# Kernel optimization log

Measured on AMD Instinct MI355X. Metric: run time of the kernel, lower is better.

Reference implementation:

```python
import jax, jax.numpy as jnp
import numpy as np

N_TOKEN = 100000
D = 1024  # d_embed == d_model == d_proj
CUTOFFS = [0, 20000, 60000, 100000]  # cutoff_ends
N_SEQ = 2048


def setup_inputs() -> dict:
    key = jax.random.key(0)
    ks = jax.random.split(key, 20)
    w = lambda k, s: jax.random.normal(k, s, dtype=jnp.float32) * 0.02
    return {
        "x": jax.random.randint(ks[0], (N_SEQ,), 0, N_TOKEN),
        "labels": jax.random.randint(ks[1], (N_SEQ,), 0, N_TOKEN),
        # adaptive embedding tables (d_emb_i = 1024 / 4**i) and projections [d_proj, d_emb_i]
        "emb_w0": w(ks[2], (20000, 1024)),
        "emb_w1": w(ks[3], (40000, 256)),
        "emb_w2": w(ks[4], (40000, 64)),
        "emb_proj0": w(ks[5], (1024, 1024)),
        "emb_proj1": w(ks[6], (1024, 256)),
        "emb_proj2": w(ks[7], (1024, 64)),
        # adaptive softmax output layers + projections
        "out_w0": w(ks[8], (20000, 1024)),
        "out_b0": jnp.zeros((20000,), jnp.float32),
        "out_w1": w(ks[9], (40000, 256)),
        "out_b1": jnp.zeros((40000,), jnp.float32),
        "out_w2": w(ks[10], (40000, 64)),
        "out_b2": jnp.zeros((40000,), jnp.float32),
        "out_proj0": w(ks[11], (1024, 1024)),
        "out_proj1": w(ks[12], (1024, 256)),
        "out_proj2": w(ks[13], (1024, 64)),
        # cluster head tokens (one per tail cluster)
        "cluster_w": w(ks[14], (2, 1024)),
        "cluster_b": jnp.zeros((2,), jnp.float32),
    }


def _forward(x, labels,
             emb_w0, emb_w1, emb_w2, emb_proj0, emb_proj1, emb_proj2,
             out_w0, out_b0, out_w1, out_b1, out_w2, out_b2,
             out_proj0, out_proj1, out_proj2, cluster_w, cluster_b):
    scale = jnp.asarray(D ** 0.5, jnp.float32)
    # AdaptiveEmbedding (div_val>1): per-cluster embed -> project to d_proj, scatter by range.
    # Equivalent vectorized form: build the full projected table once, then gather.
    table = jnp.concatenate([
        emb_w0 @ emb_proj0.T,   # [20000, D]
        emb_w1 @ emb_proj1.T,   # [40000, D]
        emb_w2 @ emb_proj2.T,   # [40000, D]
    ], axis=0)                   # [N_TOKEN, D]
    hidden = table[x] * scale    # [N, D]

    n = hidden.shape[0]
    rows = jnp.arange(n)

    # Head: cluster-0 vocab + one logit per tail cluster.
    head_w = jnp.concatenate([out_w0, cluster_w], axis=0)   # [20002, D]
    head_b = jnp.concatenate([out_b0, cluster_b], axis=0)   # [20002]
    head_logit = (hidden @ out_proj0) @ head_w.T + head_b   # [N, 20002]
    head_lp = jax.nn.log_softmax(head_logit, axis=-1)
    head_size = head_lp.shape[1]

    # Cluster 0: direct lookup in the head.
    lp0 = head_lp[rows, jnp.clip(labels, 0, CUTOFFS[1] - 1)]

    # Tail clusters: dense per-cluster log-softmax, gathered at shifted target,
    # plus the head cluster-token logprob (original TXL uses column -i).
    def tail(w, b, proj, i):
        l, r = CUTOFFS[i], CUTOFFS[i + 1]
        tail_lp = jax.nn.log_softmax((hidden @ proj) @ w.T + b, axis=-1)  # [N, r-l]
        t = jnp.clip(labels - l, 0, r - l - 1)
        return head_lp[:, head_size - i] + tail_lp[rows, t]

    lp1 = tail(out_w1, out_b1, out_proj1, 1)
    lp2 = tail(out_w2, out_b2, out_proj2, 2)

    logprob = jnp.where(labels < CUTOFFS[1], lp0,
               jnp.where(labels < CUTOFFS[2], lp1, lp2))
    return -logprob  # nll, [N]


def reference(x, labels,
              emb_w0, emb_w1, emb_w2, emb_proj0, emb_proj1, emb_proj2,
              out_w0, out_b0, out_w1, out_b1, out_w2, out_b2,
              out_proj0, out_proj1, out_proj2, cluster_w, cluster_b):
    return _forward(x, labels,
                    emb_w0, emb_w1, emb_w2, emb_proj0, emb_proj1, emb_proj2,
                    out_w0, out_b0, out_w1, out_b1, out_w2, out_b2,
                    out_proj0, out_proj1, out_proj2, cluster_w, cluster_b)
```

## Files before the change

kernel.cpp:

```cpp
#include <hip/hip_runtime.h>

typedef _Float16 f16x8 __attribute__((ext_vector_type(8)));
typedef _Float16 f16x4 __attribute__((ext_vector_type(4)));
typedef float f32x4 __attribute__((ext_vector_type(4)));
typedef int i32x4 __attribute__((ext_vector_type(4)));
typedef int i32x8 __attribute__((ext_vector_type(8)));
typedef unsigned char u8;

#define DEVI __device__ __forceinline__

constexpr int NROWS = 2048;
constexpr int HEADV = 20002;
constexpr int HEADP = 20480;
constexpr int NCBH  = 160;
constexpr int PSTH  = 160;
constexpr int VT    = 40000;
constexpr int VTP   = 40320;
constexpr int NCBT  = 315;
constexpr int PSTT  = 320;

DEVI void glds16(const void* g, void* l) {
  __builtin_amdgcn_global_load_lds((const __attribute__((address_space(1))) unsigned int*)g,
                                   (__attribute__((address_space(3))) unsigned int*)l,
                                   16, 0, 0);
}

#define SIG(r) (((r) >> 1) & 7)
DEVI int swzb(int b, int r) {
  return (b & ~127) | ((((b >> 4) & 7) ^ SIG(r)) << 4) | (b & 15);
}

DEVI unsigned int to_e4m3(float f) {
  unsigned u = __float_as_uint(f);
  unsigned s = (u >> 24) & 0x80u;
  float a = fabsf(f);
  if (!(a < 448.f)) return s | 0x7E;
  if (a < 0.00097656f) return s;
  int exp = (int)((u >> 23) & 0xFF) - 127;
  int qexp = exp < -6 ? -6 : exp;
  int n = __float2int_rn(a * exp2f((float)(3 - qexp)));
  if (n >= 16) { qexp++; n = 8; }
  return s | (unsigned)(n < 8 ? n : (((qexp + 7) << 3) | (n - 8)));
}

DEVI float fr8(unsigned b) {
  unsigned e = (b >> 3) & 15u, m = b & 7u;
  float v;
  if (e) v = __uint_as_float(((e + 120u) << 23) | (m << 20));
  else   v = (float)m * 0.001953125f;
  return (b & 0x80u) ? -v : v;
}

__global__ void prep_par(const int* __restrict__ x, const int* __restrict__ labels,
                         int* cl, int* headcol, int* tailpos, int* pos1, int* pos2,
                         int* L1, int* L2, int* T0, int* T1, int* T2, int* counts)
{
  int n = blockIdx.x * 256 + threadIdx.x;
  int l = labels[n];
  int c = l < 20000 ? 0 : (l < 60000 ? 1 : 2);
  cl[n] = c;
  headcol[n] = c == 0 ? l : (c == 1 ? 20001 : 20000);
  tailpos[n] = c == 1 ? l - 20000 : (c == 2 ? l - 60000 : 0);
  if (c == 1) { int s = atomicAdd(&counts[0], 1); pos1[n] = s; L1[s] = n; }
  else if (c == 2) { int s = atomicAdd(&counts[1], 1); pos2[n] = s; L2[s] = n; }
  int t = x[n];
  int tc = t < 20000 ? 0 : (t < 60000 ? 1 : 2);
  int s = atomicAdd(&counts[2 + tc], 1);
  (tc == 0 ? T0 : tc == 1 ? T1 : T2)[s] = n;
}

constexpr int PB_A = HEADP * 1024 / 8 / 256;
constexpr int PB_B = PB_A + VTP * 256 / 8 / 256;
constexpr int PB_C = PB_B + VTP * 128 / 8 / 256;
constexpr int PB_D = PB_C + 1024;
constexpr int PB_E = PB_D + 256;
constexpr int PB_F = PB_E + 64;
constexpr int PB_G = PB_F + 1024;
constexpr int PB_H = PB_G + 256;
constexpr int PB_I = PB_H + 128;

DEVI void cvt_f16(const float* src, _Float16* dst, int vb, int tid) {
  int g = vb * 256 + tid;
  float4 v = *(const float4*)(src + (size_t)g * 4);
  f16x4 o = {(_Float16)v.x, (_Float16)v.y, (_Float16)v.z, (_Float16)v.w};
  *(f16x4*)(dst + (size_t)g * 4) = o;
}

DEVI void tr32(const float* in, _Float16* out, int C, int bx, int by, int tid) {
  __shared__ float tile[32][33];
  int c0 = bx * 32, r0 = by * 32;
  int tx = tid & 31, ty = tid >> 5;
  for (int i = 0; i < 4; i++) {
    int c = c0 + tx; int r = r0 + ty + i * 8;
    tile[ty + i * 8][tx] = (c < C) ? in[(size_t)r * C + c] : 0.f;
  }
  __syncthreads();
  for (int i = 0; i < 4; i++)
    out[(size_t)(c0 + ty + i * 8) * 1024 + r0 + tx] = (_Float16)tile[tx][ty + i * 8];
}

DEVI unsigned long pack8(const float* v) {
  unsigned long p = 0;
  #pragma unroll
  for (int j = 0; j < 8; j++) p |= (unsigned long)to_e4m3(v[j] * 64.f) << (8 * j);
  return p;
}

__global__ void fused_pack(const float* __restrict__ out_w0, const float* __restrict__ out_b0,
                           const float* __restrict__ cluster_w, const float* __restrict__ cluster_b,
                           const float* __restrict__ out_w1, const float* __restrict__ out_b1,
                           const float* __restrict__ out_w2, const float* __restrict__ out_b2,
                           const float* __restrict__ emb_proj0, const float* __restrict__ emb_proj1,
                           const float* __restrict__ emb_proj2,
                           const float* __restrict__ out_proj0, const float* __restrict__ out_proj1,
                           const float* __restrict__ out_proj2,
                           u8* headw, float* headb,
                           u8* w1q, float* b1p, u8* w2q, float* b2p,
                           _Float16* ep0f, _Float16* ep1f, _Float16* ep2f,
                           _Float16* op0T, _Float16* op1T, _Float16* op2T,
                           int* lists, int* counts)
{
  int bid = blockIdx.x, tid = threadIdx.x;
  int zi = bid * 256 + tid;
  if (zi < 5 * 2048) lists[zi] = 0;
  if (bid == 41 && tid < 8) counts[tid] = 0;
  if (bid < PB_A) {
    int g = bid * 256 + tid;
    int r = g >> 7, sl = g & 127;
    float v[8] = {};
    if (r < 20000) {
      *(float4*)v = *(const float4*)(out_w0 + (size_t)r * 1024 + sl * 8);
      *(float4*)(v + 4) = *(const float4*)(out_w0 + (size_t)r * 1024 + sl * 8 + 4);
    } else if (r < 20002) {
      *(float4*)v = *(const float4*)(cluster_w + (size_t)(r - 20000) * 1024 + sl * 8);
      *(float4*)(v + 4) = *(const float4*)(cluster_w + (size_t)(r - 20000) * 1024 + sl * 8 + 4);
    }
    *(unsigned long*)(headw + (size_t)r * 1024 + swzb(sl * 8, r)) = pack8(v);
    if (g < HEADP) headb[g] = g < 20000 ? out_b0[g] : (g < HEADV ? cluster_b[g - 20000] : -1e30f);
  } else if (bid < PB_B) {
    int g = (bid - PB_A) * 256 + tid;
    int r = g >> 5, sl = g & 31;
    float v[8] = {};
    if (r < VT) {
      *(float4*)v = *(const float4*)(out_w1 + (size_t)r * 256 + sl * 8);
      *(float4*)(v + 4) = *(const float4*)(out_w1 + (size_t)r * 256 + sl * 8 + 4);
    }
    *(unsigned long*)(w1q + (size_t)r * 256 + swzb(sl * 8, r)) = pack8(v);
    if (g < VTP) b1p[g] = g < VT ? out_b1[g] : -1e30f;
  } else if (bid < PB_C) {
    int g = (bid - PB_B) * 256 + tid;
    int r = g >> 4, sl = g & 15;
    float v[8] = {};
    if (r < VT && sl < 8) {
      *(float4*)v = *(const float4*)(out_w2 + (size_t)r * 64 + sl * 8);
      *(float4*)(v + 4) = *(const float4*)(out_w2 + (size_t)r * 64 + sl * 8 + 4);
    }
    *(unsigned long*)(w2q + (size_t)r * 128 + swzb(sl * 8, r)) = pack8(v);
    if (g < VTP) b2p[g] = g < VT ? out_b2[g] : -1e30f;
  } else if (bid < PB_D) { cvt_f16(emb_proj0, ep0f, bid - PB_C, tid); }
  else if (bid < PB_E) { cvt_f16(emb_proj1, ep1f, bid - PB_D, tid); }
  else if (bid < PB_F) { cvt_f16(emb_proj2, ep2f, bid - PB_E, tid); }
  else if (bid < PB_G) { int l = bid - PB_F; tr32(out_proj0, op0T, 1024, l & 31, l >> 5, tid); }
  else if (bid < PB_H) { int l = bid - PB_G; tr32(out_proj1, op1T, 256, l & 7, l >> 3, tid); }
  else                 { int l = bid - PB_H; tr32(out_proj2, op2T, 64, l & 3, l >> 2, tid); }
}

DEVI void gat(const float* emb, const int* x, const int* list, _Float16* dst,
              int tbase, int vmax, int log2E, int vb, int tid) {
  int g = vb * 256 + tid;
  int r = g >> (log2E - 2);
  int e4 = (g & ((1 << (log2E - 2)) - 1)) << 2;
  int n = list[r];
  int tl = x[n] - tbase;
  tl = tl < 0 ? 0 : (tl >= vmax ? vmax - 1 : tl);
  float4 v = *(const float4*)(emb + ((size_t)tl << log2E) + e4);
  f16x4 o = {(_Float16)(v.x * 32.f), (_Float16)(v.y * 32.f),
             (_Float16)(v.z * 32.f), (_Float16)(v.w * 32.f)};
  *(f16x4*)(dst + ((size_t)r << log2E) + e4) = o;
}

__global__ void fused_gather(const float* __restrict__ emb_w0, const float* __restrict__ emb_w1,
                             const float* __restrict__ emb_w2, const int* __restrict__ x,
                             const int* __restrict__ T0, const int* __restrict__ T1,
                             const int* __restrict__ T2,
                             _Float16* E0, _Float16* E1, _Float16* E2)
{
  int bid = blockIdx.x, tid = threadIdx.x;
  if (bid < 2048)      gat(emb_w0, x, T0, E0, 0, 20000, 10, bid, tid);
  else if (bid < 2560) gat(emb_w1, x, T1, E1, 20000, 40000, 8, bid - 2048, tid);
  else                 gat(emb_w2, x, T2, E2, 60000, 40000, 6, bid - 2560, tid);
}

struct Seg128 {
  const _Float16* A; int lda;
  const _Float16* Wm; int ldw;
  _Float16* C; int ldc; int Nvalid;
  u8* Cq; int ldq;
  const int* amap; const int* cmap; const int* cnt;
  int K; int nblk;
};

DEVI void gemm128_body(const Seg128& s, int rb, int cb) {
  int valid = s.cnt ? *s.cnt : NROWS;
  if (rb * 128 >= valid) return;
  __shared__ __attribute__((aligned(16))) _Float16 As[128 * 32];
  __shared__ __attribute__((aligned(16))) _Float16 Ws[128 * 32];
  int tid = threadIdx.x;
  int lane = tid & 63, wid = tid >> 6;
  int wr = wid >> 1, wc = wid & 1;
  int sr = wid * 32 + (lane >> 2);
  int arow0 = rb * 128 + sr, arow1 = arow0 + 16;
  if (s.amap) { arow0 = s.amap[arow0]; arow1 = s.amap[arow1]; }
  int ko = (lane & 3) * 8;
  const _Float16* ag0 = s.A + (size_t)arow0 * s.lda + ko;
  const _Float16* ag1 = s.A + (size_t)arow1 * s.lda + ko;
  const _Float16* wg0 = s.Wm + (size_t)(cb * 128 + sr) * s.ldw + ko;
  const _Float16* wg1 = wg0 + (size_t)16 * s.ldw;
  _Float16* as0 = As + (wid * 32) * 32;
  _Float16* as1 = as0 + 16 * 32;
  _Float16* ws0 = Ws + (wid * 32) * 32;
  _Float16* ws1 = ws0 + 16 * 32;
  f32x4 acc[4][4] = {};
  int lr = lane & 15, lk = (lane >> 4) * 8;
  const int nk = s.K >> 5;
  for (int kt = 0; kt < nk; ++kt) {
    int kofs = kt * 32;
    glds16(ag0 + kofs, as0);
    glds16(ag1 + kofs, as1);
    glds16(wg0 + kofs, ws0);
    glds16(wg1 + kofs, ws1);
    __syncthreads();
    f16x8 af[4], bf[4];
    #pragma unroll
    for (int mi = 0; mi < 4; mi++)
      af[mi] = *(const f16x8*)(As + (wr * 64 + mi * 16 + lr) * 32 + lk);
    #pragma unroll
    for (int ni = 0; ni < 4; ni++)
      bf[ni] = *(const f16x8*)(Ws + (wc * 64 + ni * 16 + lr) * 32 + lk);
    #pragma unroll
    for (int mi = 0; mi < 4; mi++)
      #pragma unroll
      for (int ni = 0; ni < 4; ni++)
        acc[mi][ni] = __builtin_amdgcn_mfma_f32_16x16x32_f16(af[mi], bf[ni], acc[mi][ni], 0, 0, 0);
    __syncthreads();
  }
  #pragma unroll
  for (int mi = 0; mi < 4; mi++) {
    #pragma unroll
    for (int j = 0; j < 4; j++) {
      int rl = wr * 64 + mi * 16 + (lane >> 4) * 4 + j;
      int rg = rb * 128 + rl;
      if (rg >= valid) continue;
      int orow = s.cmap ? s.cmap[rg] : rg;
      #pragma unroll
      for (int ni = 0; ni < 4; ni++) {
        int col = cb * 128 + wc * 64 + ni * 16 + (lane & 15);
        if (col < s.Nvalid) {
          float v = acc[mi][ni][j];
          s.C[(size_t)orow * s.ldc + col] = (_Float16)v;
          if (s.Cq) s.Cq[(size_t)orow * s.ldq + swzb(col, orow)] = (u8)to_e4m3(v * 8.f);
        }
      }
    }
  }
}

__global__ __launch_bounds__(256)
void gemm128_multi(Seg128 s0, Seg128 s1, Seg128 s2) {
  int b = blockIdx.x;
  if (b < s0.nblk)                    { gemm128_body(s0, b & 15, b >> 4); }
  else if (b < s0.nblk + s1.nblk)     { b -= s0.nblk; gemm128_body(s1, b & 15, b >> 4); }
  else                                { b -= s0.nblk + s1.nblk; gemm128_body(s2, b & 15, b >> 4); }
}

struct SegL {
  const u8* A; const u8* W; const float* bias; const int* cnt;
  float* pm; float* ps; int pstride; int K; int nrb; int nblk;
};

__global__ __launch_bounds__(256, 3)
void gemm_lse8_multi(SegL s0, SegL s1, SegL s2)
{
  __shared__ __attribute__((aligned(16))) u8 As[16384];
  __shared__ __attribute__((aligned(16))) u8 Ws[16384];

  int b = blockIdx.x;
  SegL s;
  if (b < s0.nblk) s = s0;
  else if (b < s0.nblk + s1.nblk) { s = s1; b -= s0.nblk; }
  else { s = s2; b -= s0.nblk + s1.nblk; }

  int q = s.nblk >> 3;
  int w = (b & 7) * q + (b >> 3);
  int rb = w % s.nrb, cb = w / s.nrb;
  int valid = s.cnt ? *s.cnt : NROWS;
  if (rb * 128 >= valid) return;

  const int K = s.K;
  int tid = threadIdx.x;
  int lane = tid & 63, wid = tid >> 6;
  int wr = wid >> 1, wc = wid & 1;
  int lr = lane & 15, g = lane >> 4;

  const u8* aS[4]; const u8* bS[4]; int dL[4];
  #pragma unroll
  for (int i = 0; i < 4; ++i) {
    int c = tid + i * 256;
    int r = c >> 3, j = c & 7;
    aS[i] = s.A + (size_t)(rb * 128 + r) * K + j * 16;
    bS[i] = s.W + (size_t)((size_t)cb * 128 + r) * K + j * 16;
    dL[i] = c * 16;
  }

  int sig = SIG(lr);
  int p0 = ((2 * g + 0) ^ sig) << 4;
  int p1 = ((2 * g + 1) ^ sig) << 4;
  int arow = (wr * 64 + lr) * 128;
  int brow = (wc * 64 + lr) * 128;

  f32x4 acc[4][4] = {};
  const int nk = K >> 7;

  union UV { i32x8 v; i32x4 h[2]; };
  for (int kt = 0; kt < nk; ++kt) {
    int k0 = kt * 128;
    #pragma unroll
    for (int i = 0; i < 4; ++i) glds16(aS[i] + k0, As + dL[i]);
    #pragma unroll
    for (int i = 0; i < 4; ++i) glds16(bS[i] + k0, Ws + dL[i]);
    __syncthreads();
    i32x8 bq[4];
    #pragma unroll
    for (int ni = 0; ni < 4; ++ni) {
      UV bv;
      const u8* bp = Ws + brow + ni * 2048;
      bv.h[0] = *(const i32x4*)(bp + p0);
      bv.h[1] = *(const i32x4*)(bp + p1);
      bq[ni] = bv.v;
    }
    #pragma unroll
    for (int mi = 0; mi < 4; ++mi) {
      UV av;
      const u8* ap = As + arow + mi * 2048;
      av.h[0] = *(const i32x4*)(ap + p0);
      av.h[1] = *(const i32x4*)(ap + p1);
      #pragma unroll
      for (int ni = 0; ni < 4; ++ni)
        acc[mi][ni] = __builtin_amdgcn_mfma_scale_f32_16x16x128_f8f6f4(
                        av.v, bq[ni], acc[mi][ni], 0, 0, 0, 127, 0, 127);
    }
    __syncthreads();
  }

  float* lm = (float*)As;
  float* lsm = lm + 256;
  float bv4[4];
  #pragma unroll
  for (int ni = 0; ni < 4; ++ni) bv4[ni] = s.bias[cb * 128 + wc * 64 + ni * 16 + lr];
  constexpr float INV = 1.f / 512.f;
  #pragma unroll
  for (int mi = 0; mi < 4; ++mi) {
    #pragma unroll
    for (int j = 0; j < 4; ++j) {
      float v0 = acc[mi][0][j] * INV + bv4[0];
      float v1 = acc[mi][1][j] * INV + bv4[1];
      float v2 = acc[mi][2][j] * INV + bv4[2];
      float v3 = acc[mi][3][j] * INV + bv4[3];
      float m = fmaxf(fmaxf(v0, v1), fmaxf(v2, v3));
      #pragma unroll
      for (int d = 1; d < 16; d <<= 1) m = fmaxf(m, __shfl_xor(m, d));
      float sm = __expf(v0 - m) + __expf(v1 - m) + __expf(v2 - m) + __expf(v3 - m);
      #pragma unroll
      for (int d = 1; d < 16; d <<= 1) sm += __shfl_xor(sm, d);
      if (lr == 0) {
        int row = wr * 64 + mi * 16 + g * 4 + j;
        lm[wc * 128 + row] = m; lsm[wc * 128 + row] = sm;
      }
    }
  }
  __syncthreads();
  if (tid < 128) {
    float m0 = lm[tid], m1 = lm[128 + tid];
    float M = fmaxf(m0, m1);
    float S = lsm[tid] * __expf(m0 - M) + lsm[128 + tid] * __expf(m1 - M);
    int gr = rb * 128 + tid;
    s.pm[(size_t)gr * s.pstride + cb] = M;
    s.ps[(size_t)gr * s.pstride + cb] = S;
  }
}

DEVI float lsew(const float* m, const float* s, int nb, int lane) {
  float M = -3e38f;
  for (int i = lane; i < nb; i += 64) M = fmaxf(M, m[i]);
  #pragma unroll
  for (int d = 1; d < 64; d <<= 1) M = fmaxf(M, __shfl_xor(M, d));
  float S = 0.f;
  for (int i = lane; i < nb; i += 64) S += s[i] * __expf(m[i] - M);
  #pragma unroll
  for (int d = 1; d < 64; d <<= 1) S += __shfl_xor(S, d);
  return M + __logf(S);
}

__global__ void finish_kernel(const _Float16* __restrict__ ph0, const u8* __restrict__ headw,
                              const float* __restrict__ headb,
                              const _Float16* __restrict__ ph1c, const u8* __restrict__ w1q,
                              const float* __restrict__ b1p,
                              const _Float16* __restrict__ ph2c, const u8* __restrict__ w2q,
                              const float* __restrict__ b2p,
                              const int* __restrict__ headcol, const int* __restrict__ tailpos,
                              const int* __restrict__ pos1, const int* __restrict__ pos2,
                              const int* __restrict__ cl,
                              const float* __restrict__ pmh, const float* __restrict__ psh,
                              const float* __restrict__ pm1, const float* __restrict__ ps1,
                              const float* __restrict__ pm2, const float* __restrict__ ps2,
                              float* __restrict__ out)
{
  int n = blockIdx.x;
  int tid = threadIdx.x, lane = tid & 63, wid = tid >> 6;
  __shared__ float sh[6];
  int c = cl[n];
  constexpr float IW = 1.f / 64.f;
  if (wid == 0) {
    int hc = headcol[n];
    const f16x8* a = (const f16x8*)(ph0 + (size_t)n * 1024 + lane * 16);
    float s = 0.f;
    #pragma unroll
    for (int u = 0; u < 2; u++) {
      unsigned long wq = *(const unsigned long*)(headw + (size_t)hc * 1024 + swzb(lane * 16 + u * 8, hc));
      f16x8 av = a[u];
      #pragma unroll
      for (int j = 0; j < 8; j++) s += (float)av[j] * fr8((unsigned)(wq >> (8 * j)) & 0xFFu);
    }
    #pragma unroll
    for (int d = 1; d < 64; d <<= 1) s += __shfl_xor(s, d);
    if (lane == 0) sh[0] = s * IW + headb[hc];
  } else if (wid == 1 && c == 1) {
    int p = pos1[n], t = tailpos[n];
    f16x4 av = *(const f16x4*)(ph1c + (size_t)p * 256 + lane * 4);
    const u8* ww = w1q + (size_t)t * 256 + swzb(lane * 4, t);
    float s = (float)av[0] * fr8(ww[0]) + (float)av[1] * fr8(ww[1])
            + (float)av[2] * fr8(ww[2]) + (float)av[3] * fr8(ww[3]);
    #pragma unroll
    for (int d = 1; d < 64; d <<= 1) s += __shfl_xor(s, d);
    float l = lsew(pm1 + (size_t)p * PSTT, ps1 + (size_t)p * PSTT, NCBT, lane);
    if (lane == 0) { sh[1] = s * IW + b1p[t]; sh[4] = l; }
  } else if (wid == 2 && c == 2) {
    int p = pos2[n], t = tailpos[n];
    const _Float16* a = ph2c + (size_t)p * 128 + lane * 2;
    const u8* ww = w2q + (size_t)t * 128 + swzb(lane * 2, t);
    float s = (float)a[0] * fr8(ww[0]) + (float)a[1] * fr8(ww[1]);
    #pragma unroll
    for (int d = 1; d < 64; d <<= 1) s += __shfl_xor(s, d);
    float l = lsew(pm2 + (size_t)p * PSTT, ps2 + (size_t)p * PSTT, NCBT, lane);
    if (lane == 0) { sh[2] = s * IW + b2p[t]; sh[5] = l; }
  } else if (wid == 3) {
    float l = lsew(pmh + (size_t)n * PSTH, psh + (size_t)n * PSTH, NCBH, lane);
    if (lane == 0) sh[3] = l;
  }
  __syncthreads();
  if (tid == 0) {
    float nll = sh[3] - sh[0];
    if (c == 1)      nll += sh[4] - sh[1];
    else if (c == 2) nll += sh[5] - sh[2];
    out[n] = nll;
  }
}

extern "C" void kernel_launch(void* const* d_in, const int* in_sizes, int n_in,
                              void* d_out, int out_size, void* d_ws, size_t ws_size,
                              hipStream_t stream)
{
  const int*   x         = (const int*)d_in[0];
  const int*   labels    = (const int*)d_in[1];
  const float* emb_w0    = (const float*)d_in[2];
  const float* emb_w1    = (const float*)d_in[3];
  const float* emb_w2    = (const float*)d_in[4];
  const float* emb_proj0 = (const float*)d_in[5];
  const float* emb_proj1 = (const float*)d_in[6];
  const float* emb_proj2 = (const float*)d_in[7];
  const float* out_w0    = (const float*)d_in[8];
  const float* out_b0    = (const float*)d_in[9];
  const float* out_w1    = (const float*)d_in[10];
  const float* out_b1    = (const float*)d_in[11];
  const float* out_w2    = (const float*)d_in[12];
  const float* out_b2    = (const float*)d_in[13];
  const float* out_proj0 = (const float*)d_in[14];
  const float* out_proj1 = (const float*)d_in[15];
  const float* out_proj2 = (const float*)d_in[16];
  const float* cluster_w = (const float*)d_in[17];
  const float* cluster_b = (const float*)d_in[18];
  float* out = (float*)d_out;

  char* ws = (char*)d_ws;
  size_t off = 0;
  auto alloc = [&](size_t bytes) -> void* {
    void* p = ws + off;
    off = (off + bytes + 255) & ~(size_t)255;
    return p;
  };
  u8*    headw = (u8*)alloc((size_t)HEADP * 1024);
  float* headb = (float*)alloc((size_t)HEADP * 4);
  u8*    w1q   = (u8*)alloc((size_t)VTP * 256);
  float* b1p   = (float*)alloc((size_t)VTP * 4);
  u8*    w2q   = (u8*)alloc((size_t)VTP * 128);
  float* b2p   = (float*)alloc((size_t)VTP * 4);
  _Float16* ep0f = (_Float16*)alloc((size_t)1024 * 1024 * 2);
  _Float16* ep1f = (_Float16*)alloc((size_t)1024 * 256 * 2);
  _Float16* ep2f = (_Float16*)alloc((size_t)1024 * 64 * 2);
  _Float16* op0T = (_Float16*)alloc((size_t)1024 * 1024 * 2);
  _Float16* op1T = (_Float16*)alloc((size_t)256 * 1024 * 2);
  _Float16* op2T = (_Float16*)alloc((size_t)128 * 1024 * 2);
  _Float16* E0   = (_Float16*)alloc((size_t)NROWS * 1024 * 2);
  _Float16* E1   = (_Float16*)alloc((size_t)NROWS * 256 * 2);
  _Float16* E2   = (_Float16*)alloc((size_t)NROWS * 64 * 2);
  _Float16* hid  = (_Float16*)alloc((size_t)NROWS * 1024 * 2);
  _Float16* ph0  = (_Float16*)alloc((size_t)NROWS * 1024 * 2);
  u8*       ph0q = (u8*)alloc((size_t)NROWS * 1024);
  _Float16* ph1c = (_Float16*)alloc((size_t)NROWS * 256 * 2);
  u8*       ph1q = (u8*)alloc((size_t)NROWS * 256);
  _Float16* ph2c = (_Float16*)alloc((size_t)NROWS * 128 * 2);
  u8*       ph2q = (u8*)alloc((size_t)NROWS * 128);
  float* pmh = (float*)alloc((size_t)NROWS * PSTH * 4);
  float* psh = (float*)alloc((size_t)NROWS * PSTH * 4);
  float* pm1 = (float*)alloc((size_t)NROWS * PSTT * 4);
  float* ps1 = (float*)alloc((size_t)NROWS * PSTT * 4);
  float* pm2 = (float*)alloc((size_t)NROWS * PSTT * 4);
  float* ps2 = (float*)alloc((size_t)NROWS * PSTT * 4);
  int* lists = (int*)alloc(5 * NROWS * 4);
  int* L1 = lists;
  int* L2 = lists + 2048;
  int* T0 = lists + 4096;
  int* T1 = lists + 6144;
  int* T2 = lists + 8192;
  int* counts  = (int*)alloc(16 * 4);
  int* cl      = (int*)alloc(NROWS * 4);
  int* headcol = (int*)alloc(NROWS * 4);
  int* tailpos = (int*)alloc(NROWS * 4);
  int* pos1    = (int*)alloc(NROWS * 4);
  int* pos2    = (int*)alloc(NROWS * 4);
  (void)ws_size; (void)in_sizes; (void)n_in; (void)out_size;

  fused_pack<<<PB_I, 256, 0, stream>>>(out_w0, out_b0, cluster_w, cluster_b,
                                       out_w1, out_b1, out_w2, out_b2,
                                       emb_proj0, emb_proj1, emb_proj2,
                                       out_proj0, out_proj1, out_proj2,
                                       headw, headb, w1q, b1p, w2q, b2p,
                                       ep0f, ep1f, ep2f, op0T, op1T, op2T,
                                       lists, counts);

  prep_par<<<8, 256, 0, stream>>>(x, labels, cl, headcol, tailpos, pos1, pos2,
                                  L1, L2, T0, T1, T2, counts);

  fused_gather<<<2688, 256, 0, stream>>>(emb_w0, emb_w1, emb_w2, x, T0, T1, T2, E0, E1, E2);

  Seg128 h0 = {E0, 1024, ep0f, 1024, hid, 1024, 1024, nullptr, 0, nullptr, T0, counts + 2, 1024, 128};
  Seg128 h1 = {E1, 256,  ep1f, 256,  hid, 1024, 1024, nullptr, 0, nullptr, T1, counts + 3, 256,  128};
  Seg128 h2 = {E2, 64,   ep2f, 64,   hid, 1024, 1024, nullptr, 0, nullptr, T2, counts + 4, 64,   128};
  gemm128_multi<<<384, 256, 0, stream>>>(h0, h1, h2);

  Seg128 p0 = {hid, 1024, op0T, 1024, ph0,  1024, 1024, ph0q, 1024, nullptr, nullptr, nullptr,   1024, 128};
  Seg128 p1 = {hid, 1024, op1T, 1024, ph1c, 256,  256,  ph1q, 256,  L1,      nullptr, counts + 0, 1024, 32};
  Seg128 p2 = {hid, 1024, op2T, 1024, ph2c, 128,  128,  ph2q, 128,  L2,      nullptr, counts + 1, 1024, 16};
  gemm128_multi<<<176, 256, 0, stream>>>(p0, p1, p2);

  SegL l0 = {ph0q, headw, headb, nullptr,    pmh, psh, PSTH, 1024, 16, 16 * NCBH};
  SegL l1 = {ph1q, w1q,   b1p,   counts + 0, pm1, ps1, PSTT, 256,  8,  8 * NCBT};
  SegL l2 = {ph2q, w2q,   b2p,   counts + 1, pm2, ps2, PSTT, 128,  8,  8 * NCBT};
  gemm_lse8_multi<<<16 * NCBH + 16 * NCBT, 256, 0, stream>>>(l0, l1, l2);

  finish_kernel<<<NROWS, 256, 0, stream>>>(ph0, headw, headb, ph1c, w1q, b1p,
                                           ph2c, w2q, b2p, headcol, tailpos, pos1, pos2, cl,
                                           pmh, psh, pm1, ps1, pm2, ps2, out);
}
```

Baseline: 255.4 us.

## Widen fused LSE GEMM tile to 256x128 and store partials column-major

The fp8 logits-plus-logsumexp GEMM now has each block cover 256 rows by 128 vocab columns instead of 128x128. Each of the four waves computes a full 64x128 strip, so the cross-wave LDS reduction goes away and per-wave max/sum partials are written straight to global memory in a [column-block][row] layout. The goal is to halve how often the large vocab weight matrix is re-read and to drop an LDS sync and combine step. In exchange it doubles accumulators and LDS per block, lowers occupancy from 3 to 2 blocks, and makes the finish kernel read partials with a 2048-element stride. The LDS swizzle signature also changes from (r>>1)&7 to r&7 to spread the 16-byte fragment reads across more banks.

```diff
diff --git a/kernel.cpp b/kernel.cpp
--- a/kernel.cpp
+++ b/kernel.cpp
@@ -13,11 +13,9 @@
 constexpr int HEADV = 20002;
 constexpr int HEADP = 20480;
 constexpr int NCBH  = 160;
-constexpr int PSTH  = 160;
 constexpr int VT    = 40000;
 constexpr int VTP   = 40320;
 constexpr int NCBT  = 315;
-constexpr int PSTT  = 320;
 
 DEVI void glds16(const void* g, void* l) {
   __builtin_amdgcn_global_load_lds((const __attribute__((address_space(1))) unsigned int*)g,
@@ -25,7 +23,7 @@
                                    16, 0, 0);
 }
 
-#define SIG(r) (((r) >> 1) & 7)
+#define SIG(r) ((r) & 7)
 DEVI int swzb(int b, int r) {
   return (b & ~127) | ((((b >> 4) & 7) ^ SIG(r)) << 4) | (b & 15);
 }
@@ -275,13 +273,13 @@
 
 struct SegL {
   const u8* A; const u8* W; const float* bias; const int* cnt;
-  float* pm; float* ps; int pstride; int K; int nrb; int nblk;
+  float* pm; float* ps; int K; int nblk;
 };
 
-__global__ __launch_bounds__(256, 3)
+__global__ __launch_bounds__(256, 2)
 void gemm_lse8_multi(SegL s0, SegL s1, SegL s2)
 {
-  __shared__ __attribute__((aligned(16))) u8 As[16384];
+  __shared__ __attribute__((aligned(16))) u8 As[32768];
   __shared__ __attribute__((aligned(16))) u8 Ws[16384];
 
   int b = blockIdx.x;
@@ -292,46 +290,50 @@
 
   int q = s.nblk >> 3;
   int w = (b & 7) * q + (b >> 3);
-  int rb = w % s.nrb, cb = w / s.nrb;
+  int rb = w & 7, cb = w >> 3;
   int valid = s.cnt ? *s.cnt : NROWS;
-  if (rb * 128 >= valid) return;
+  if (rb * 256 >= valid) return;
 
   const int K = s.K;
   int tid = threadIdx.x;
   int lane = tid & 63, wid = tid >> 6;
-  int wr = wid >> 1, wc = wid & 1;
   int lr = lane & 15, g = lane >> 4;
 
-  const u8* aS[4]; const u8* bS[4]; int dL[4];
+  const u8* aS[8]; int dA[8];
+  #pragma unroll
+  for (int i = 0; i < 8; ++i) {
+    int c = tid + i * 256;
+    aS[i] = s.A + (size_t)(rb * 256 + (c >> 3)) * K + (c & 7) * 16;
+    dA[i] = c * 16;
+  }
+  const u8* bS[4]; int dB[4];
   #pragma unroll
   for (int i = 0; i < 4; ++i) {
     int c = tid + i * 256;
-    int r = c >> 3, j = c & 7;
-    aS[i] = s.A + (size_t)(rb * 128 + r) * K + j * 16;
-    bS[i] = s.W + (size_t)((size_t)cb * 128 + r) * K + j * 16;
-    dL[i] = c * 16;
+    bS[i] = s.W + (size_t)((size_t)cb * 128 + (c >> 3)) * K + (c & 7) * 16;
+    dB[i] = c * 16;
   }
 
   int sig = SIG(lr);
   int p0 = ((2 * g + 0) ^ sig) << 4;
   int p1 = ((2 * g + 1) ^ sig) << 4;
-  int arow = (wr * 64 + lr) * 128;
-  int brow = (wc * 64 + lr) * 128;
-
-  f32x4 acc[4][4] = {};
+  int arow = (wid * 64 + lr) * 128;
+  int brow = lr * 128;
+
+  f32x4 acc[4][8] = {};
   const int nk = K >> 7;
 
   union UV { i32x8 v; i32x4 h[2]; };
   for (int kt = 0; kt < nk; ++kt) {
     int k0 = kt * 128;
     #pragma unroll
-    for (int i = 0; i < 4; ++i) glds16(aS[i] + k0, As + dL[i]);
-    #pragma unroll
-    for (int i = 0; i < 4; ++i) glds16(bS[i] + k0, Ws + dL[i]);
+    for (int i = 0; i < 8; ++i) glds16(aS[i] + k0, As + dA[i]);
+    #pragma unroll
+    for (int i = 0; i < 4; ++i) glds16(bS[i] + k0, Ws + dB[i]);
     __syncthreads();
-    i32x8 bq[4];
-    #pragma unroll
-    for (int ni = 0; ni < 4; ++ni) {
+    i32x8 bq[8];
+    #pragma unroll
+    for (int ni = 0; ni < 8; ++ni) {
       UV bv;
       const u8* bp = Ws + brow + ni * 2048;
       bv.h[0] = *(const i32x4*)(bp + p0);
@@ -345,57 +347,50 @@
       av.h[0] = *(const i32x4*)(ap + p0);
       av.h[1] = *(const i32x4*)(ap + p1);
       #pragma unroll
-      for (int ni = 0; ni < 4; ++ni)
+      for (int ni = 0; ni < 8; ++ni)
         acc[mi][ni] = __builtin_amdgcn_mfma_scale_f32_16x16x128_f8f6f4(
                         av.v, bq[ni], acc[mi][ni], 0, 0, 0, 127, 0, 127);
     }
     __syncthreads();
   }
 
-  float* lm = (float*)As;
-  float* lsm = lm + 256;
-  float bv4[4];
-  #pragma unroll
-  for (int ni = 0; ni < 4; ++ni) bv4[ni] = s.bias[cb * 128 + wc * 64 + ni * 16 + lr];
+  float bv8[8];
+  #pragma unroll
+  for (int ni = 0; ni < 8; ++ni) bv8[ni] = s.bias[cb * 128 + ni * 16 + lr];
   constexpr float INV = 1.f / 512.f;
   #pragma unroll
   for (int mi = 0; mi < 4; ++mi) {
     #pragma unroll
     for (int j = 0; j < 4; ++j) {
-      float v0 = acc[mi][0][j] * INV + bv4[0];
-      float v1 = acc[mi][1][j] * INV + bv4[1];
-      float v2 = acc[mi][2][j] * INV + bv4[2];
-      float v3 = acc[mi][3][j] * INV + bv4[3];
-      float m = fmaxf(fmaxf(v0, v1), fmaxf(v2, v3));
+      float vv[8]; float m = -3e38f;
+      #pragma unroll
+      for (int ni = 0; ni < 8; ++ni) {
+        vv[ni] = acc[mi][ni][j] * INV + bv8[ni];
+        m = fmaxf(m, vv[ni]);
+      }
       #pragma unroll
       for (int d = 1; d < 16; d <<= 1) m = fmaxf(m, __shfl_xor(m, d));
-      float sm = __expf(v0 - m) + __expf(v1 - m) + __expf(v2 - m) + __expf(v3 - m);
+      float sm = 0.f;
+      #pragma unroll
+      for (int ni = 0; ni < 8; ++ni) sm += __expf(vv[ni] - m);
       #pragma unroll
       for (int d = 1; d < 16; d <<= 1) sm += __shfl_xor(sm, d);
       if (lr == 0) {
-        int row = wr * 64 + mi * 16 + g * 4 + j;
-        lm[wc * 128 + row] = m; lsm[wc * 128 + row] = sm;
+        int row = rb * 256 + wid * 64 + mi * 16 + g * 4 + j;
+        s.pm[(size_t)cb * 2048 + row] = m;
+        s.ps[(size_t)cb * 2048 + row] = sm;
       }
     }
-  }
-  __syncthreads();
-  if (tid < 128) {
-    float m0 = lm[tid], m1 = lm[128 + tid];
-    float M = fmaxf(m0, m1);
-    float S = lsm[tid] * __expf(m0 - M) + lsm[128 + tid] * __expf(m1 - M);
-    int gr = rb * 128 + tid;
-    s.pm[(size_t)gr * s.pstride + cb] = M;
-    s.ps[(size_t)gr * s.pstride + cb] = S;
   }
 }
 
 DEVI float lsew(const float* m, const float* s, int nb, int lane) {
   float M = -3e38f;
-  for (int i = lane; i < nb; i += 64) M = fmaxf(M, m[i]);
+  for (int i = lane; i < nb; i += 64) M = fmaxf(M, m[(size_t)i * 2048]);
   #pragma unroll
   for (int d = 1; d < 64; d <<= 1) M = fmaxf(M, __shfl_xor(M, d));
   float S = 0.f;
-  for (int i = lane; i < nb; i += 64) S += s[i] * __expf(m[i] - M);
+  for (int i = lane; i < nb; i += 64) S += s[(size_t)i * 2048] * __expf(m[(size_t)i * 2048] - M);
   #pragma unroll
   for (int d = 1; d < 64; d <<= 1) S += __shfl_xor(S, d);
   return M + __logf(S);
@@ -442,7 +437,7 @@
             + (float)av[2] * fr8(ww[2]) + (float)av[3] * fr8(ww[3]);
     #pragma unroll
     for (int d = 1; d < 64; d <<= 1) s += __shfl_xor(s, d);
-    float l = lsew(pm1 + (size_t)p * PSTT, ps1 + (size_t)p * PSTT, NCBT, lane);
+    float l = lsew(pm1 + p, ps1 + p, NCBT, lane);
     if (lane == 0) { sh[1] = s * IW + b1p[t]; sh[4] = l; }
   } else if (wid == 2 && c == 2) {
     int p = pos2[n], t = tailpos[n];
@@ -451,10 +446,10 @@
     float s = (float)a[0] * fr8(ww[0]) + (float)a[1] * fr8(ww[1]);
     #pragma unroll
     for (int d = 1; d < 64; d <<= 1) s += __shfl_xor(s, d);
-    float l = lsew(pm2 + (size_t)p * PSTT, ps2 + (size_t)p * PSTT, NCBT, lane);
+    float l = lsew(pm2 + p, ps2 + p, NCBT, lane);
     if (lane == 0) { sh[2] = s * IW + b2p[t]; sh[5] = l; }
   } else if (wid == 3) {
-    float l = lsew(pmh + (size_t)n * PSTH, psh + (size_t)n * PSTH, NCBH, lane);
+    float l = lsew(pmh + n, psh + n, NCBH, lane);
     if (lane == 0) sh[3] = l;
   }
   __syncthreads();
@@ -520,12 +515,12 @@
   u8*       ph1q = (u8*)alloc((size_t)NROWS * 256);
   _Float16* ph2c = (_Float16*)alloc((size_t)NROWS * 128 * 2);
   u8*       ph2q = (u8*)alloc((size_t)NROWS * 128);
-  float* pmh = (float*)alloc((size_t)NROWS * PSTH * 4);
-  float* psh = (float*)alloc((size_t)NROWS * PSTH * 4);
-  float* pm1 = (float*)alloc((size_t)NROWS * PSTT * 4);
-  float* ps1 = (float*)alloc((size_t)NROWS * PSTT * 4);
-  float* pm2 = (float*)alloc((size_t)NROWS * PSTT * 4);
-  float* ps2 = (float*)alloc((size_t)NROWS * PSTT * 4);
+  float* pmh = (float*)alloc((size_t)NCBH * 2048 * 4);
+  float* psh = (float*)alloc((size_t)NCBH * 2048 * 4);
+  float* pm1 = (float*)alloc((size_t)NCBT * 2048 * 4);
+  float* ps1 = (float*)alloc((size_t)NCBT * 2048 * 4);
+  float* pm2 = (float*)alloc((size_t)NCBT * 2048 * 4);
+  float* ps2 = (float*)alloc((size_t)NCBT * 2048 * 4);
   int* lists = (int*)alloc(5 * NROWS * 4);
   int* L1 = lists;
   int* L2 = lists + 2048;
@@ -563,10 +558,10 @@
   Seg128 p2 = {hid, 1024, op2T, 1024, ph2c, 128,  128,  ph2q, 128,  L2,      nullptr, counts + 1, 1024, 16};
   gemm128_multi<<<176, 256, 0, stream>>>(p0, p1, p2);
 
-  SegL l0 = {ph0q, headw, headb, nullptr,    pmh, psh, PSTH, 1024, 16, 16 * NCBH};
-  SegL l1 = {ph1q, w1q,   b1p,   counts + 0, pm1, ps1, PSTT, 256,  8,  8 * NCBT};
-  SegL l2 = {ph2q, w2q,   b2p,   counts + 1, pm2, ps2, PSTT, 128,  8,  8 * NCBT};
-  gemm_lse8_multi<<<16 * NCBH + 16 * NCBT, 256, 0, stream>>>(l0, l1, l2);
+  SegL l0 = {ph0q, headw, headb, nullptr,    pmh, psh, 1024, 8 * NCBH};
+  SegL l1 = {ph1q, w1q,   b1p,   counts + 0, pm1, ps1, 256,  8 * NCBT};
+  SegL l2 = {ph2q, w2q,   b2p,   counts + 1, pm2, ps2, 128,  8 * NCBT};
+  gemm_lse8_multi<<<8 * NCBH + 16 * NCBT, 256, 0, stream>>>(l0, l1, l2);
 
   finish_kernel<<<NROWS, 256, 0, stream>>>(ph0, headw, headb, ph1c, w1q, b1p,
                                            ph2c, w2q, b2p, headcol, tailpos, pos1, pos2, cl,
```

After: 252.1 us (median of 2 runs). About the same (-1.3%).
